# Kernel tuning notes

Measured on AMD Instinct MI355X. Metric: run time of the kernel, lower is better.

## Reference

```python
import jax, jax.numpy as jnp
import numpy as np

N_EDGES = 4096
HIDDEN = 256
EDGE_DIM = 128
NUM_HEADS = 4
NUM_GRAPHS = 64


def setup_inputs() -> dict:
    key0 = jax.random.key(0)
    ks = jax.random.split(key0, 10)
    s = 0.02
    inp = {
        "query": jax.random.normal(ks[0], (N_EDGES, HIDDEN), jnp.float32),
        "key": jax.random.normal(ks[1], (N_EDGES, EDGE_DIM), jnp.float32),
        "value": jax.random.normal(ks[2], (N_EDGES, EDGE_DIM), jnp.float32),
        "edge_graph_index": jnp.sort(
            jax.random.randint(ks[3], (N_EDGES,), 0, NUM_GRAPHS)
        ),
        # edge_proj: Linear(edge_context_dim -> hidden_dim)
        "w_edge": jax.random.normal(ks[4], (HIDDEN, EDGE_DIM), jnp.float32) * s,
        "b_edge": jnp.zeros((HIDDEN,), jnp.float32),
        # nn.MultiheadAttention packed in-projection [3H, H] and bias [3H]
        "w_in": jax.random.normal(ks[5], (3 * HIDDEN, HIDDEN), jnp.float32) * s,
        "b_in": jnp.zeros((3 * HIDDEN,), jnp.float32),
        # out_proj: Linear(hidden -> hidden)
        "w_out": jax.random.normal(ks[6], (HIDDEN, HIDDEN), jnp.float32) * s,
        "b_out": jnp.zeros((HIDDEN,), jnp.float32),
    }
    return inp


def reference(query, key, value, edge_graph_index,
              w_edge, b_edge, w_in, b_in, w_out, b_out):
    # Segment-wise cross attention == block-diagonal masked attention over all edges.
    N, H = query.shape
    nh = NUM_HEADS
    dh = H // nh

    # edge feature projection (applied to both key and value, as in the module)
    K = key @ w_edge.T + b_edge      # [N, H]
    V = value @ w_edge.T + b_edge    # [N, H]

    wq, wk, wv = jnp.split(w_in, 3, axis=0)
    bq, bk, bv = jnp.split(b_in, 3)
    Qh = (query @ wq.T + bq).reshape(N, nh, dh)
    Kh = (K @ wk.T + bk).reshape(N, nh, dh)
    Vh = (V @ wv.T + bv).reshape(N, nh, dh)

    scale = 1.0 / jnp.sqrt(jnp.asarray(dh, query.dtype))
    scores = jnp.einsum("nhd,mhd->hnm", Qh, Kh) * scale  # [nh, N, N]

    # attention only within the same graph segment
    same_graph = edge_graph_index[:, None] == edge_graph_index[None, :]  # [N, N]
    neg = jnp.finfo(scores.dtype).min
    scores = jnp.where(same_graph[None, :, :], scores, neg)

    attn = jax.nn.softmax(scores, axis=-1)                 # [nh, N, N]
    out = jnp.einsum("hnm,mhd->nhd", attn, Vh).reshape(N, H)
    out = out @ w_out.T + b_out
    return query + out
```

## Files before the change

kernel.cpp:

```cpp
#include <hip/hip_runtime.h>

#define N_EDGES 4096
#define HIDDEN  256
#define EDGE_DIM 128
#define NUM_HEADS 4
#define NUM_GRAPHS 64
#define DH 64

typedef __attribute__((ext_vector_type(8))) short short8;
typedef __attribute__((ext_vector_type(4))) float f32x4;

__device__ __forceinline__ unsigned short f2bf(float f) {
  unsigned u = __builtin_bit_cast(unsigned, f);
  u += 0x7FFF + ((u >> 16) & 1);
  return (unsigned short)(u >> 16);
}

struct GemmArgs {
  const float* A;
  const float* W;
  const float* bias;
  const float* res;
  float* C;
  int K;
};

__global__ __launch_bounds__(256) void gemm_mfma(GemmArgs g0, GemmArgs g1, GemmArgs g2) {
  GemmArgs ga = (blockIdx.z == 0) ? g0 : (blockIdx.z == 1 ? g1 : g2);
  const int t = threadIdx.x;
  const int m0 = blockIdx.x * 64, n0 = blockIdx.y * 64;
  __shared__ unsigned short As[64 * 40];
  __shared__ unsigned short Ws[64 * 40];
  const int r = t >> 2, kg = t & 3;
  const int lane = t & 63, w = t >> 6;
  const int quad = lane >> 4, l16 = lane & 15;
  const int wm = (w >> 1) * 32, wn = (w & 1) * 32;
  const int K = ga.K;
  f32x4 acc[2][2] = {};
  const float* pa = ga.A + (size_t)(m0 + r) * K + kg * 8;
  const float* pw = ga.W + (size_t)(n0 + r) * K + kg * 8;
  float4 a0 = *(const float4*)(pa);
  float4 a1 = *(const float4*)(pa + 4);
  float4 w0 = *(const float4*)(pw);
  float4 w1 = *(const float4*)(pw + 4);
  for (int kc = 0; kc < K; kc += 32) {
    float4 na0, na1, nw0, nw1;
    if (kc + 32 < K) {
      na0 = *(const float4*)(pa + kc + 32);
      na1 = *(const float4*)(pa + kc + 36);
      nw0 = *(const float4*)(pw + kc + 32);
      nw1 = *(const float4*)(pw + kc + 36);
    }
    __syncthreads();
    short8 av, wv;
    av[0] = (short)f2bf(a0.x); av[1] = (short)f2bf(a0.y);
    av[2] = (short)f2bf(a0.z); av[3] = (short)f2bf(a0.w);
    av[4] = (short)f2bf(a1.x); av[5] = (short)f2bf(a1.y);
    av[6] = (short)f2bf(a1.z); av[7] = (short)f2bf(a1.w);
    wv[0] = (short)f2bf(w0.x); wv[1] = (short)f2bf(w0.y);
    wv[2] = (short)f2bf(w0.z); wv[3] = (short)f2bf(w0.w);
    wv[4] = (short)f2bf(w1.x); wv[5] = (short)f2bf(w1.y);
    wv[6] = (short)f2bf(w1.z); wv[7] = (short)f2bf(w1.w);
    *(short8*)&As[r * 40 + kg * 8] = av;
    *(short8*)&Ws[r * 40 + kg * 8] = wv;
    __syncthreads();
    short8 af0 = *(const short8*)&As[(wm + l16) * 40 + quad * 8];
    short8 af1 = *(const short8*)&As[(wm + 16 + l16) * 40 + quad * 8];
    short8 bf0 = *(const short8*)&Ws[(wn + l16) * 40 + quad * 8];
    short8 bf1 = *(const short8*)&Ws[(wn + 16 + l16) * 40 + quad * 8];
    acc[0][0] = __builtin_amdgcn_mfma_f32_16x16x32_bf16(af0, bf0, acc[0][0], 0, 0, 0);
    acc[0][1] = __builtin_amdgcn_mfma_f32_16x16x32_bf16(af0, bf1, acc[0][1], 0, 0, 0);
    acc[1][0] = __builtin_amdgcn_mfma_f32_16x16x32_bf16(af1, bf0, acc[1][0], 0, 0, 0);
    acc[1][1] = __builtin_amdgcn_mfma_f32_16x16x32_bf16(af1, bf1, acc[1][1], 0, 0, 0);
    a0 = na0; a1 = na1; w0 = nw0; w1 = nw1;
  }
#pragma unroll
  for (int j = 0; j < 2; ++j) {
    const int col = n0 + wn + j * 16 + l16;
    const float bj = ga.bias[col];
#pragma unroll
    for (int i = 0; i < 2; ++i) {
#pragma unroll
      for (int reg = 0; reg < 4; ++reg) {
        const int row = m0 + wm + i * 16 + quad * 4 + reg;
        float v = acc[i][j][reg] + bj;
        if (ga.res) v += ga.res[(size_t)row * HIDDEN + col];
        ga.C[(size_t)row * HIDDEN + col] = v;
      }
    }
  }
}

__device__ __forceinline__ int lbound(const int* __restrict__ a, int n, int v) {
  int lo = 0, hi = n;
  while (lo < hi) { int mid = (lo + hi) >> 1; if (a[mid] < v) lo = mid + 1; else hi = mid; }
  return lo;
}

__global__ __launch_bounds__(128) void combine_w(const float* __restrict__ w_in,
                                                 const float* __restrict__ b_in,
                                                 const float* __restrict__ w_edge,
                                                 const float* __restrict__ b_edge,
                                                 const int* __restrict__ g,
                                                 float* Wk, float* bk, float* Wv, float* bv,
                                                 int* segStart) {
  const int o = blockIdx.x;
  const int kv = blockIdx.y;
  const int j = threadIdx.x;
  if (o == 0 && kv == 0 && j <= NUM_GRAPHS)
    segStart[j] = lbound(g, N_EDGES, j);
  const float* wrow = w_in + (size_t)(HIDDEN + kv * HIDDEN + o) * HIDDEN;
  __shared__ float wr[HIDDEN];
  wr[j] = wrow[j]; wr[j + 128] = wrow[j + 128];
  __syncthreads();
  float acc = 0.f;
#pragma unroll 8
  for (int m = 0; m < HIDDEN; ++m) acc += wr[m] * w_edge[(size_t)m * EDGE_DIM + j];
  (kv ? Wv : Wk)[(size_t)o * EDGE_DIM + j] = acc;
  float bacc = wr[j] * b_edge[j] + wr[j + 128] * b_edge[j + 128];
  __shared__ float red[128];
  red[j] = bacc;
  __syncthreads();
  if (j < 64) {
    float v = red[j] + red[j + 64];
#pragma unroll
    for (int off = 32; off; off >>= 1) v += __shfl_xor(v, off);
    if (j == 0) (kv ? bv : bk)[o] = v + b_in[HIDDEN + kv * HIDDEN + o];
  }
}

__global__ __launch_bounds__(256) void attn_segment(const float* __restrict__ Qh,
                                                    const float* __restrict__ Kh,
                                                    const float* __restrict__ Vh,
                                                    const int* __restrict__ segStart,
                                                    float* __restrict__ out) {
  const int graph = blockIdx.x, h = blockIdx.y, zg = blockIdx.z;
  const int segLo = segStart[graph];
  const int segHi = segStart[graph + 1];
  const int segLen = segHi - segLo;
  const int t = threadIdx.x, lane = t & 63, w = t >> 6;
  __shared__ float Qs[16][68], Ks[64][68], Vs[64][68];
  __shared__ float Ps[4][64][4];
  const float scale = 0.125f;
  const int r0 = w * 4;

  for (int chunk = zg; chunk * 16 < segLen; chunk += 8) {
    const int row0 = segLo + chunk * 16;
    const int rows = min(16, segHi - row0);
    __syncthreads();
    { int r = t >> 4, d4 = (t & 15) * 4;
      if (r < rows)
        *(float4*)&Qs[r][d4] = *(const float4*)(Qh + (size_t)(row0 + r) * HIDDEN + h * DH + d4); }

    float accv[4] = {0.f, 0.f, 0.f, 0.f}, lsum[4] = {0.f, 0.f, 0.f, 0.f};

    for (int c0 = segLo; c0 < segHi; c0 += 64) {
      const int tc = min(64, segHi - c0);
      __syncthreads();
#pragma unroll
      for (int it = 0; it < 4; ++it) {
        int s = t + it * 256; int j = s >> 4; int d4 = (s & 15) * 4;
        if (j < tc) {
          *(float4*)&Ks[j][d4] = *(const float4*)(Kh + (size_t)(c0 + j) * HIDDEN + h * DH + d4);
          *(float4*)&Vs[j][d4] = *(const float4*)(Vh + (size_t)(c0 + j) * HIDDEN + h * DH + d4);
        }
      }
      __syncthreads();
      float4 kreg[16];
#pragma unroll
      for (int d4 = 0; d4 < 16; ++d4) kreg[d4] = *(const float4*)&Ks[lane][d4 * 4];
      float p[4];
#pragma unroll
      for (int r = 0; r < 4; ++r) {
        float s = 0.f;
#pragma unroll
        for (int d4 = 0; d4 < 16; ++d4) {
          float4 q = *(const float4*)&Qs[r0 + r][d4 * 4];
          s += q.x * kreg[d4].x + q.y * kreg[d4].y + q.z * kreg[d4].z + q.w * kreg[d4].w;
        }
        p[r] = (lane < tc && r0 + r < rows) ? __expf(s * scale) : 0.f;
        lsum[r] += p[r];
      }
      float4 p4; p4.x = p[0]; p4.y = p[1]; p4.z = p[2]; p4.w = p[3];
      *(float4*)&Ps[w][lane][0] = p4;
      __asm__ volatile("s_waitcnt lgkmcnt(0)" ::: "memory");
      for (int j = 0; j < tc; ++j) {
        const float v = Vs[j][lane];
        float4 pj = *(const float4*)&Ps[w][j][0];
        accv[0] += pj.x * v; accv[1] += pj.y * v;
        accv[2] += pj.z * v; accv[3] += pj.w * v;
      }
    }
#pragma unroll
    for (int off = 32; off; off >>= 1)
#pragma unroll
      for (int r = 0; r < 4; ++r) lsum[r] += __shfl_xor(lsum[r], off);
#pragma unroll
    for (int r = 0; r < 4; ++r)
      if (r0 + r < rows)
        out[(size_t)(row0 + r0 + r) * HIDDEN + h * DH + lane] = accv[r] / lsum[r];
  }
}

extern "C" void kernel_launch(void* const* d_in, const int* in_sizes, int n_in,
                              void* d_out, int out_size, void* d_ws, size_t ws_size,
                              hipStream_t stream) {
  const float* query  = (const float*)d_in[0];
  const float* key    = (const float*)d_in[1];
  const float* value  = (const float*)d_in[2];
  const int*   gidx   = (const int*)d_in[3];
  const float* w_edge = (const float*)d_in[4];
  const float* b_edge = (const float*)d_in[5];
  const float* w_in   = (const float*)d_in[6];
  const float* b_in   = (const float*)d_in[7];
  const float* w_out  = (const float*)d_in[8];
  const float* b_out  = (const float*)d_in[9];
  float* out = (float*)d_out;
  float* ws = (float*)d_ws;

  float* Wk = ws;
  float* Wv = ws + 32768;
  float* bk = ws + 65536;
  float* bv = ws + 65792;
  int*   segStart = (int*)(ws + 66048);
  float* Qh = ws + 66176;
  float* Kh = Qh + 1048576;
  float* Vh = Kh + 1048576;
  float* ao = Vh + 1048576;

  combine_w<<<dim3(256, 2), 128, 0, stream>>>(w_in, b_in, w_edge, b_edge, gidx,
                                              Wk, bk, Wv, bv, segStart);

  GemmArgs gq{query, w_in, b_in, nullptr, Qh, 256};
  GemmArgs gk{key,   Wk,   bk,   nullptr, Kh, 128};
  GemmArgs gv{value, Wv,   bv,   nullptr, Vh, 128};
  gemm_mfma<<<dim3(64, 4, 3), 256, 0, stream>>>(gq, gk, gv);

  attn_segment<<<dim3(NUM_GRAPHS, NUM_HEADS, 8), 256, 0, stream>>>(Qh, Kh, Vh, segStart, ao);

  GemmArgs go{ao, w_out, b_out, query, out, 256};
  gemm_mfma<<<dim3(64, 4, 1), 256, 0, stream>>>(go, go, go);
}
```

Baseline: 129.1 us.

## Store intermediates in bf16, chain projections, fuse output projection into attention

Removes the weight-combination kernel. The edge projection now runs as its own GEMM, followed by a second GEMM for the K/V in-projection. All intermediates are stored as bf16 to halve their memory traffic. The attention kernel now loops over all heads inside a block and applies the output projection plus residual with MFMA directly from shared memory, which removes the separate out-projection launch and the fp32 attention-output buffer. The trade-offs: grid parallelism drops from graph×head×8 to graph×8 blocks, each block does four times the serial attention work, and the chained bf16 projection adds rounding error.

```diff
diff --git a/kernel.cpp b/kernel.cpp
--- a/kernel.cpp
+++ b/kernel.cpp
@@ -15,18 +15,28 @@
   u += 0x7FFF + ((u >> 16) & 1);
   return (unsigned short)(u >> 16);
 }
-
-struct GemmArgs {
-  const float* A;
-  const float* W;
-  const float* bias;
-  const float* res;
-  float* C;
-  int K;
-};
-
-__global__ __launch_bounds__(256) void gemm_mfma(GemmArgs g0, GemmArgs g1, GemmArgs g2) {
-  GemmArgs ga = (blockIdx.z == 0) ? g0 : (blockIdx.z == 1 ? g1 : g2);
+__device__ __forceinline__ float bf2f(unsigned short u) {
+  return __builtin_bit_cast(float, (unsigned)u << 16);
+}
+__device__ __forceinline__ short8 cvt8(float4 x, float4 y) {
+  short8 v;
+  v[0] = (short)f2bf(x.x); v[1] = (short)f2bf(x.y);
+  v[2] = (short)f2bf(x.z); v[3] = (short)f2bf(x.w);
+  v[4] = (short)f2bf(y.x); v[5] = (short)f2bf(y.y);
+  v[6] = (short)f2bf(y.z); v[7] = (short)f2bf(y.w);
+  return v;
+}
+
+__device__ __forceinline__ int lbound(const int* __restrict__ a, int n, int v) {
+  int lo = 0, hi = n;
+  while (lo < hi) { int mid = (lo + hi) >> 1; if (a[mid] < v) lo = mid + 1; else hi = mid; }
+  return lo;
+}
+
+template<bool ABF>
+__device__ __forceinline__ void gemm_core(const void* Ap, const float* W,
+                                          const float* bias, unsigned short* C,
+                                          const int K) {
   const int t = threadIdx.x;
   const int m0 = blockIdx.x * 64, n0 = blockIdx.y * 64;
   __shared__ unsigned short As[64 * 40];
@@ -35,34 +45,25 @@
   const int lane = t & 63, w = t >> 6;
   const int quad = lane >> 4, l16 = lane & 15;
   const int wm = (w >> 1) * 32, wn = (w & 1) * 32;
-  const int K = ga.K;
   f32x4 acc[2][2] = {};
-  const float* pa = ga.A + (size_t)(m0 + r) * K + kg * 8;
-  const float* pw = ga.W + (size_t)(n0 + r) * K + kg * 8;
-  float4 a0 = *(const float4*)(pa);
-  float4 a1 = *(const float4*)(pa + 4);
-  float4 w0 = *(const float4*)(pw);
-  float4 w1 = *(const float4*)(pw + 4);
+  const float* pw = W + (size_t)(n0 + r) * K + kg * 8;
+  float4 w0 = *(const float4*)(pw), w1 = *(const float4*)(pw + 4);
+  const unsigned short* pa16 = (const unsigned short*)Ap + (size_t)(m0 + r) * K + kg * 8;
+  const float* pa32 = (const float*)Ap + (size_t)(m0 + r) * K + kg * 8;
+  short8 a16; float4 a0, a1;
+  if (ABF) a16 = *(const short8*)pa16;
+  else { a0 = *(const float4*)pa32; a1 = *(const float4*)(pa32 + 4); }
   for (int kc = 0; kc < K; kc += 32) {
-    float4 na0, na1, nw0, nw1;
+    short8 na16; float4 na0, na1, nw0, nw1;
     if (kc + 32 < K) {
-      na0 = *(const float4*)(pa + kc + 32);
-      na1 = *(const float4*)(pa + kc + 36);
-      nw0 = *(const float4*)(pw + kc + 32);
-      nw1 = *(const float4*)(pw + kc + 36);
-    }
-    __syncthreads();
-    short8 av, wv;
-    av[0] = (short)f2bf(a0.x); av[1] = (short)f2bf(a0.y);
-    av[2] = (short)f2bf(a0.z); av[3] = (short)f2bf(a0.w);
-    av[4] = (short)f2bf(a1.x); av[5] = (short)f2bf(a1.y);
-    av[6] = (short)f2bf(a1.z); av[7] = (short)f2bf(a1.w);
-    wv[0] = (short)f2bf(w0.x); wv[1] = (short)f2bf(w0.y);
-    wv[2] = (short)f2bf(w0.z); wv[3] = (short)f2bf(w0.w);
-    wv[4] = (short)f2bf(w1.x); wv[5] = (short)f2bf(w1.y);
-    wv[6] = (short)f2bf(w1.z); wv[7] = (short)f2bf(w1.w);
+      if (ABF) na16 = *(const short8*)(pa16 + kc + 32);
+      else { na0 = *(const float4*)(pa32 + kc + 32); na1 = *(const float4*)(pa32 + kc + 36); }
+      nw0 = *(const float4*)(pw + kc + 32); nw1 = *(const float4*)(pw + kc + 36);
+    }
+    __syncthreads();
+    short8 av = ABF ? a16 : cvt8(a0, a1);
     *(short8*)&As[r * 40 + kg * 8] = av;
-    *(short8*)&Ws[r * 40 + kg * 8] = wv;
+    *(short8*)&Ws[r * 40 + kg * 8] = cvt8(w0, w1);
     __syncthreads();
     short8 af0 = *(const short8*)&As[(wm + l16) * 40 + quad * 8];
     short8 af1 = *(const short8*)&As[(wm + 16 + l16) * 40 + quad * 8];
@@ -72,75 +73,67 @@
     acc[0][1] = __builtin_amdgcn_mfma_f32_16x16x32_bf16(af0, bf1, acc[0][1], 0, 0, 0);
     acc[1][0] = __builtin_amdgcn_mfma_f32_16x16x32_bf16(af1, bf0, acc[1][0], 0, 0, 0);
     acc[1][1] = __builtin_amdgcn_mfma_f32_16x16x32_bf16(af1, bf1, acc[1][1], 0, 0, 0);
-    a0 = na0; a1 = na1; w0 = nw0; w1 = nw1;
+    a16 = na16; a0 = na0; a1 = na1; w0 = nw0; w1 = nw1;
   }
 #pragma unroll
   for (int j = 0; j < 2; ++j) {
     const int col = n0 + wn + j * 16 + l16;
-    const float bj = ga.bias[col];
+    const float bj = bias[col];
 #pragma unroll
     for (int i = 0; i < 2; ++i) {
 #pragma unroll
       for (int reg = 0; reg < 4; ++reg) {
         const int row = m0 + wm + i * 16 + quad * 4 + reg;
-        float v = acc[i][j][reg] + bj;
-        if (ga.res) v += ga.res[(size_t)row * HIDDEN + col];
-        ga.C[(size_t)row * HIDDEN + col] = v;
+        C[(size_t)row * HIDDEN + col] = f2bf(acc[i][j][reg] + bj);
       }
     }
   }
 }
 
-__device__ __forceinline__ int lbound(const int* __restrict__ a, int n, int v) {
-  int lo = 0, hi = n;
-  while (lo < hi) { int mid = (lo + hi) >> 1; if (a[mid] < v) lo = mid + 1; else hi = mid; }
-  return lo;
-}
-
-__global__ __launch_bounds__(128) void combine_w(const float* __restrict__ w_in,
-                                                 const float* __restrict__ b_in,
-                                                 const float* __restrict__ w_edge,
-                                                 const float* __restrict__ b_edge,
-                                                 const int* __restrict__ g,
-                                                 float* Wk, float* bk, float* Wv, float* bv,
-                                                 int* segStart) {
-  const int o = blockIdx.x;
-  const int kv = blockIdx.y;
-  const int j = threadIdx.x;
-  if (o == 0 && kv == 0 && j <= NUM_GRAPHS)
-    segStart[j] = lbound(g, N_EDGES, j);
-  const float* wrow = w_in + (size_t)(HIDDEN + kv * HIDDEN + o) * HIDDEN;
-  __shared__ float wr[HIDDEN];
-  wr[j] = wrow[j]; wr[j + 128] = wrow[j + 128];
-  __syncthreads();
-  float acc = 0.f;
-#pragma unroll 8
-  for (int m = 0; m < HIDDEN; ++m) acc += wr[m] * w_edge[(size_t)m * EDGE_DIM + j];
-  (kv ? Wv : Wk)[(size_t)o * EDGE_DIM + j] = acc;
-  float bacc = wr[j] * b_edge[j] + wr[j + 128] * b_edge[j + 128];
-  __shared__ float red[128];
-  red[j] = bacc;
-  __syncthreads();
-  if (j < 64) {
-    float v = red[j] + red[j + 64];
-#pragma unroll
-    for (int off = 32; off; off >>= 1) v += __shfl_xor(v, off);
-    if (j == 0) (kv ? bv : bk)[o] = v + b_in[HIDDEN + kv * HIDDEN + o];
-  }
-}
-
-__global__ __launch_bounds__(256) void attn_segment(const float* __restrict__ Qh,
-                                                    const float* __restrict__ Kh,
-                                                    const float* __restrict__ Vh,
-                                                    const int* __restrict__ segStart,
-                                                    float* __restrict__ out) {
-  const int graph = blockIdx.x, h = blockIdx.y, zg = blockIdx.z;
+__global__ __launch_bounds__(256) void proj1(const float* __restrict__ query,
+                                             const float* __restrict__ key,
+                                             const float* __restrict__ value,
+                                             const float* __restrict__ w_in,
+                                             const float* __restrict__ b_in,
+                                             const float* __restrict__ w_edge,
+                                             const float* __restrict__ b_edge,
+                                             const int* __restrict__ gidx,
+                                             unsigned short* Qh, unsigned short* Ek,
+                                             unsigned short* Ev, int* segStart) {
+  if (blockIdx.z == 0 && blockIdx.x == 0 && blockIdx.y == 0 && threadIdx.x <= NUM_GRAPHS)
+    segStart[threadIdx.x] = lbound(gidx, N_EDGES, threadIdx.x);
+  if (blockIdx.z == 0)      gemm_core<false>(query, w_in,   b_in,   Qh, 256);
+  else if (blockIdx.z == 1) gemm_core<false>(key,   w_edge, b_edge, Ek, 128);
+  else                      gemm_core<false>(value, w_edge, b_edge, Ev, 128);
+}
+
+__global__ __launch_bounds__(256) void proj2(const unsigned short* __restrict__ Ek,
+                                             const unsigned short* __restrict__ Ev,
+                                             const float* __restrict__ w_in,
+                                             const float* __restrict__ b_in,
+                                             unsigned short* Kh, unsigned short* Vh) {
+  if (blockIdx.z == 0) gemm_core<true>(Ek, w_in + 256 * HIDDEN, b_in + 256, Kh, 256);
+  else                 gemm_core<true>(Ev, w_in + 512 * HIDDEN, b_in + 512, Vh, 256);
+}
+
+__global__ __launch_bounds__(256) void attn_out(const unsigned short* __restrict__ Qh,
+                                                const unsigned short* __restrict__ Kh,
+                                                const unsigned short* __restrict__ Vh,
+                                                const int* __restrict__ segStart,
+                                                const float* __restrict__ w_out,
+                                                const float* __restrict__ b_out,
+                                                const float* __restrict__ query,
+                                                float* __restrict__ out) {
+  const int graph = blockIdx.x, zg = blockIdx.y;
   const int segLo = segStart[graph];
   const int segHi = segStart[graph + 1];
   const int segLen = segHi - segLo;
   const int t = threadIdx.x, lane = t & 63, w = t >> 6;
-  __shared__ float Qs[16][68], Ks[64][68], Vs[64][68];
+  const int quad = lane >> 4, l16 = lane & 15;
+  __shared__ float Qs[16][260];
+  __shared__ float Ks[64][68], Vs[64][68];
   __shared__ float Ps[4][64][4];
+  __shared__ float ao[16][260];
   const float scale = 0.125f;
   const int r0 = w * 4;
 
@@ -148,57 +141,97 @@
     const int row0 = segLo + chunk * 16;
     const int rows = min(16, segHi - row0);
     __syncthreads();
-    { int r = t >> 4, d4 = (t & 15) * 4;
-      if (r < rows)
-        *(float4*)&Qs[r][d4] = *(const float4*)(Qh + (size_t)(row0 + r) * HIDDEN + h * DH + d4); }
-
-    float accv[4] = {0.f, 0.f, 0.f, 0.f}, lsum[4] = {0.f, 0.f, 0.f, 0.f};
-
-    for (int c0 = segLo; c0 < segHi; c0 += 64) {
-      const int tc = min(64, segHi - c0);
-      __syncthreads();
-#pragma unroll
-      for (int it = 0; it < 4; ++it) {
-        int s = t + it * 256; int j = s >> 4; int d4 = (s & 15) * 4;
-        if (j < tc) {
-          *(float4*)&Ks[j][d4] = *(const float4*)(Kh + (size_t)(c0 + j) * HIDDEN + h * DH + d4);
-          *(float4*)&Vs[j][d4] = *(const float4*)(Vh + (size_t)(c0 + j) * HIDDEN + h * DH + d4);
-        }
-      }
-      __syncthreads();
-      float4 kreg[16];
-#pragma unroll
-      for (int d4 = 0; d4 < 16; ++d4) kreg[d4] = *(const float4*)&Ks[lane][d4 * 4];
-      float p[4];
-#pragma unroll
-      for (int r = 0; r < 4; ++r) {
-        float s = 0.f;
-#pragma unroll
-        for (int d4 = 0; d4 < 16; ++d4) {
-          float4 q = *(const float4*)&Qs[r0 + r][d4 * 4];
-          s += q.x * kreg[d4].x + q.y * kreg[d4].y + q.z * kreg[d4].z + q.w * kreg[d4].w;
-        }
-        p[r] = (lane < tc && r0 + r < rows) ? __expf(s * scale) : 0.f;
-        lsum[r] += p[r];
-      }
-      float4 p4; p4.x = p[0]; p4.y = p[1]; p4.z = p[2]; p4.w = p[3];
-      *(float4*)&Ps[w][lane][0] = p4;
-      __asm__ volatile("s_waitcnt lgkmcnt(0)" ::: "memory");
-      for (int j = 0; j < tc; ++j) {
-        const float v = Vs[j][lane];
-        float4 pj = *(const float4*)&Ps[w][j][0];
-        accv[0] += pj.x * v; accv[1] += pj.y * v;
-        accv[2] += pj.z * v; accv[3] += pj.w * v;
-      }
-    }
-#pragma unroll
-    for (int off = 32; off; off >>= 1)
-#pragma unroll
-      for (int r = 0; r < 4; ++r) lsum[r] += __shfl_xor(lsum[r], off);
-#pragma unroll
-    for (int r = 0; r < 4; ++r)
-      if (r0 + r < rows)
-        out[(size_t)(row0 + r0 + r) * HIDDEN + h * DH + lane] = accv[r] / lsum[r];
+#pragma unroll
+    for (int it = 0; it < 2; ++it) {
+      int s = t + it * 256; int r = s >> 5; int c8 = (s & 31) * 8;
+      if (r < rows) {
+        short8 q8 = *(const short8*)(Qh + (size_t)(row0 + r) * HIDDEN + c8);
+        float4 f0, f1;
+        f0.x = bf2f(q8[0]); f0.y = bf2f(q8[1]); f0.z = bf2f(q8[2]); f0.w = bf2f(q8[3]);
+        f1.x = bf2f(q8[4]); f1.y = bf2f(q8[5]); f1.z = bf2f(q8[6]); f1.w = bf2f(q8[7]);
+        *(float4*)&Qs[r][c8] = f0; *(float4*)&Qs[r][c8 + 4] = f1;
+      }
+    }
+
+    for (int h = 0; h < NUM_HEADS; ++h) {
+      float accv[4] = {0.f, 0.f, 0.f, 0.f}, lsum[4] = {0.f, 0.f, 0.f, 0.f};
+      for (int c0 = segLo; c0 < segHi; c0 += 64) {
+        const int tc = min(64, segHi - c0);
+        __syncthreads();
+#pragma unroll
+        for (int it = 0; it < 2; ++it) {
+          int s = t + it * 256; int j = s >> 3; int c8 = (s & 7) * 8;
+          if (j < tc) {
+            short8 k8 = *(const short8*)(Kh + (size_t)(c0 + j) * HIDDEN + h * DH + c8);
+            short8 v8 = *(const short8*)(Vh + (size_t)(c0 + j) * HIDDEN + h * DH + c8);
+#pragma unroll
+            for (int e = 0; e < 8; ++e) Ks[j][c8 + e] = bf2f(k8[e]);
+#pragma unroll
+            for (int e = 0; e < 8; ++e) Vs[j][c8 + e] = bf2f(v8[e]);
+          }
+        }
+        __syncthreads();
+        float4 kreg[16];
+#pragma unroll
+        for (int d4 = 0; d4 < 16; ++d4) kreg[d4] = *(const float4*)&Ks[lane][d4 * 4];
+        float p[4];
+#pragma unroll
+        for (int r = 0; r < 4; ++r) {
+          float s = 0.f;
+#pragma unroll
+          for (int d4 = 0; d4 < 16; ++d4) {
+            float4 q = *(const float4*)&Qs[r0 + r][h * DH + d4 * 4];
+            s += q.x * kreg[d4].x + q.y * kreg[d4].y + q.z * kreg[d4].z + q.w * kreg[d4].w;
+          }
+          p[r] = (lane < tc && r0 + r < rows) ? __expf(s * scale) : 0.f;
+          lsum[r] += p[r];
+        }
+        float4 p4; p4.x = p[0]; p4.y = p[1]; p4.z = p[2]; p4.w = p[3];
+        *(float4*)&Ps[w][lane][0] = p4;
+        __asm__ volatile("s_waitcnt lgkmcnt(0)" ::: "memory");
+        for (int j = 0; j < tc; ++j) {
+          const float v = Vs[j][lane];
+          float4 pj = *(const float4*)&Ps[w][j][0];
+          accv[0] += pj.x * v; accv[1] += pj.y * v;
+          accv[2] += pj.z * v; accv[3] += pj.w * v;
+        }
+      }
+#pragma unroll
+      for (int off = 32; off; off >>= 1)
+#pragma unroll
+        for (int r = 0; r < 4; ++r) lsum[r] += __shfl_xor(lsum[r], off);
+#pragma unroll
+      for (int r = 0; r < 4; ++r)
+        if (r0 + r < rows) ao[r0 + r][h * DH + lane] = accv[r] / lsum[r];
+    }
+    __syncthreads();
+
+    const int wn = w * 64;
+    f32x4 oc[4] = {};
+    for (int kc = 0; kc < HIDDEN; kc += 32) {
+      float4 a0 = *(const float4*)&ao[l16][kc + quad * 8];
+      float4 a1 = *(const float4*)&ao[l16][kc + quad * 8 + 4];
+      short8 af = cvt8(a0, a1);
+#pragma unroll
+      for (int nt = 0; nt < 4; ++nt) {
+        const float* wr = w_out + (size_t)(wn + nt * 16 + l16) * HIDDEN + kc + quad * 8;
+        short8 bf = cvt8(*(const float4*)wr, *(const float4*)(wr + 4));
+        oc[nt] = __builtin_amdgcn_mfma_f32_16x16x32_bf16(af, bf, oc[nt], 0, 0, 0);
+      }
+    }
+#pragma unroll
+    for (int nt = 0; nt < 4; ++nt) {
+      const int col = wn + nt * 16 + l16;
+      const float bj = b_out[col];
+#pragma unroll
+      for (int reg = 0; reg < 4; ++reg) {
+        const int m = quad * 4 + reg;
+        if (m < rows) {
+          const size_t idx = (size_t)(row0 + m) * HIDDEN + col;
+          out[idx] = oc[nt][reg] + bj + query[idx];
+        }
+      }
+    }
   }
 }
 
@@ -216,28 +249,17 @@
   const float* w_out  = (const float*)d_in[8];
   const float* b_out  = (const float*)d_in[9];
   float* out = (float*)d_out;
-  float* ws = (float*)d_ws;
-
-  float* Wk = ws;
-  float* Wv = ws + 32768;
-  float* bk = ws + 65536;
-  float* bv = ws + 65792;
-  int*   segStart = (int*)(ws + 66048);
-  float* Qh = ws + 66176;
-  float* Kh = Qh + 1048576;
-  float* Vh = Kh + 1048576;
-  float* ao = Vh + 1048576;
-
-  combine_w<<<dim3(256, 2), 128, 0, stream>>>(w_in, b_in, w_edge, b_edge, gidx,
-                                              Wk, bk, Wv, bv, segStart);
-
-  GemmArgs gq{query, w_in, b_in, nullptr, Qh, 256};
-  GemmArgs gk{key,   Wk,   bk,   nullptr, Kh, 128};
-  GemmArgs gv{value, Wv,   bv,   nullptr, Vh, 128};
-  gemm_mfma<<<dim3(64, 4, 3), 256, 0, stream>>>(gq, gk, gv);
-
-  attn_segment<<<dim3(NUM_GRAPHS, NUM_HEADS, 8), 256, 0, stream>>>(Qh, Kh, Vh, segStart, ao);
-
-  GemmArgs go{ao, w_out, b_out, query, out, 256};
-  gemm_mfma<<<dim3(64, 4, 1), 256, 0, stream>>>(go, go, go);
-}
+
+  int* segStart = (int*)d_ws;
+  unsigned short* Qh = (unsigned short*)((char*)d_ws + 512);
+  unsigned short* Ek = Qh + (size_t)N_EDGES * HIDDEN;
+  unsigned short* Ev = Ek + (size_t)N_EDGES * HIDDEN;
+  unsigned short* Kh = Ev + (size_t)N_EDGES * HIDDEN;
+  unsigned short* Vh = Kh + (size_t)N_EDGES * HIDDEN;
+
+  proj1<<<dim3(64, 4, 3), 256, 0, stream>>>(query, key, value, w_in, b_in,
+                                            w_edge, b_edge, gidx, Qh, Ek, Ev, segStart);
+  proj2<<<dim3(64, 4, 2), 256, 0, stream>>>(Ek, Ev, w_in, b_in, Kh, Vh);
+  attn_out<<<dim3(NUM_GRAPHS, 8), 256, 0, stream>>>(Qh, Kh, Vh, segStart,
+                                                    w_out, b_out, query, out);
+}
```

After: 144.1 us. 11.6% more time.
